# Kernel tuning notes

Hardware: AMD Instinct MI355X
Metric: run time of the kernel (lower is better)

Reference implementation:

```python
import jax, jax.numpy as jnp
import numpy as np

B, IN, OUT, NC, S = 4096, 512, 512, 64, 1


def setup_inputs() -> dict:
    key = jax.random.key(0)
    k = jax.random.split(key, 5)
    x = jax.random.normal(k[0], (B, IN), dtype=jnp.float32)
    centers = jax.random.normal(k[1], (NC, IN), dtype=jnp.float32)
    log_sigma = jnp.zeros((NC,), dtype=jnp.float32)
    coeff_mean = jax.random.normal(k[2], (IN, OUT, NC), dtype=jnp.float32) * 0.05
    coeff_log_var = jnp.full((IN, OUT, NC), -5.0, dtype=jnp.float32)
    base_weight = jax.random.normal(k[3], (IN, OUT), dtype=jnp.float32) * 0.05
    eps = jax.random.normal(k[4], (S, IN, OUT, NC), dtype=jnp.float32)
    return {"x": x, "centers": centers, "log_sigma": log_sigma,
            "coeff_mean": coeff_mean, "coeff_log_var": coeff_log_var,
            "base_weight": base_weight, "eps": eps}


def reference(x, centers, log_sigma, coeff_mean, coeff_log_var, base_weight, eps):
    # RBF basis: (B, NC). Original repeats this along in_features, but the
    # einsum 'bin,ion->bo' with an i-constant basis equals rbf @ coeffs.sum(i).
    dist_sq = jnp.sum((x[:, None, :] - centers[None, :, :]) ** 2, axis=-1)  # (B, NC)
    sigma = jnp.exp(log_sigma)  # (NC,)
    rbf = jnp.exp(-dist_sq / (2.0 * sigma ** 2 + 1e-8))  # (B, NC)

    # Sampled variational coefficients, reparameterized.
    std = jnp.exp(0.5 * coeff_log_var)
    coeffs = coeff_mean + eps * std            # (S, IN, OUT, NC)
    c_sum = coeffs.sum(axis=1)                 # (S, OUT, NC): sum over in_features
    n_samples = eps.shape[0]
    rbf_out = jnp.einsum('bn,son->bo', rbf, c_sum) / n_samples  # mean over samples

    out = rbf_out + x @ base_weight

    # KL vs N(0, 1) prior (prior_scale = 1.0): log(var/prior_var) = coeff_log_var
    var = jnp.exp(coeff_log_var)
    kl = 0.5 * jnp.sum(var + coeff_mean ** 2 - 1.0 - coeff_log_var)
    return out, kl
```

## Files before the change

kernel.cpp:

```cpp
#include <hip/hip_runtime.h>
#include <hip/hip_bf16.h>

#define B_SZ  4096
#define IN_F  512
#define OUT_F 512
#define NC    64
#define PAIRS 32768
#define TOT   (IN_F * PAIRS)
#define KTOT  (IN_F + NC)
#define RCH   32

typedef __attribute__((ext_vector_type(8))) short bf16x8;
typedef __attribute__((ext_vector_type(4))) float f32x4;

static __device__ inline unsigned short f2bf(float f) {
    __hip_bfloat16 h = __float2bfloat16(f);
    return *(unsigned short*)&h;
}

__global__ __launch_bounds__(512)
void k1_partial(const float* __restrict__ cm,
                const float* __restrict__ clv,
                const float* __restrict__ eps,
                float* __restrict__ part,
                float* __restrict__ klpart,
                int S) {
    int pb = blockIdx.x & 15;
    int rc = blockIdx.x >> 4;
    int p4 = pb * 2048 + (threadIdx.x << 2);
    float Sf = (float)S;

    f32x4 s = {0.f, 0.f, 0.f, 0.f};
    float klp = 0.f;

    for (int g = 0; g < 2; ++g) {
        size_t base = (size_t)(rc * 16 + g * 8) * PAIRS + p4;
        f32x4 M[8], LV[8], ES[8];
#pragma unroll
        for (int ii = 0; ii < 8; ++ii)
            M[ii] = __builtin_nontemporal_load((const f32x4*)(cm + base + (size_t)ii * PAIRS));
#pragma unroll
        for (int ii = 0; ii < 8; ++ii)
            LV[ii] = __builtin_nontemporal_load((const f32x4*)(clv + base + (size_t)ii * PAIRS));
#pragma unroll
        for (int ii = 0; ii < 8; ++ii)
            ES[ii] = __builtin_nontemporal_load((const f32x4*)(eps + base + (size_t)ii * PAIRS));
        for (int si = 1; si < S; ++si)
#pragma unroll
            for (int ii = 0; ii < 8; ++ii) {
                f32x4 e = __builtin_nontemporal_load(
                    (const f32x4*)(eps + (size_t)si * TOT + base + (size_t)ii * PAIRS));
                ES[ii] += e;
            }

#pragma unroll
        for (int ii = 0; ii < 8; ++ii) {
            float e1x = __expf(0.5f * LV[ii].x);
            float e1y = __expf(0.5f * LV[ii].y);
            float e1z = __expf(0.5f * LV[ii].z);
            float e1w = __expf(0.5f * LV[ii].w);
            s.x += Sf * M[ii].x + ES[ii].x * e1x;
            s.y += Sf * M[ii].y + ES[ii].y * e1y;
            s.z += Sf * M[ii].z + ES[ii].z * e1z;
            s.w += Sf * M[ii].w + ES[ii].w * e1w;
            klp += (e1x*e1x + M[ii].x*M[ii].x - 1.f - LV[ii].x);
            klp += (e1y*e1y + M[ii].y*M[ii].y - 1.f - LV[ii].y);
            klp += (e1z*e1z + M[ii].z*M[ii].z - 1.f - LV[ii].z);
            klp += (e1w*e1w + M[ii].w*M[ii].w - 1.f - LV[ii].w);
        }
    }

    *(f32x4*)(part + (size_t)rc * PAIRS + p4) = s;

    for (int off = 32; off; off >>= 1)
        klp += __shfl_down(klp, off, 64);
    __shared__ float wsum[8];
    if ((threadIdx.x & 63) == 0) wsum[threadIdx.x >> 6] = klp;
    __syncthreads();
    if (threadIdx.x == 0) {
        float t = 0.f;
#pragma unroll
        for (int i = 0; i < 8; ++i) t += wsum[i];
        klpart[blockIdx.x] = t;
    }
}

__global__ __launch_bounds__(512)
void k_mid(const float* __restrict__ x,
           const float* __restrict__ centers,
           const float* __restrict__ log_sigma,
           const float* __restrict__ part,
           const float* __restrict__ klpart,
           const float* __restrict__ bw,
           unsigned short* __restrict__ rbf,
           unsigned short* __restrict__ wct,
           unsigned short* __restrict__ xbf,
           float* __restrict__ kl_out,
           float inv_S) {
    __shared__ float shbuf[16 * 8 * 64];
    int bid = blockIdx.x, t = threadIdx.x;

    if (bid < 256) {
        float (*red)[8][64] = (float (*)[8][64])shbuf;
        int n = t & 63;
        int wu = __builtin_amdgcn_readfirstlane(t >> 6);
        int b0 = bid * 16;

        float creg[64];
#pragma unroll
        for (int q = 0; q < 16; ++q) {
            float4 v = *(const float4*)(centers + (size_t)n * IN_F + wu * 64 + q * 4);
            creg[q * 4 + 0] = v.x; creg[q * 4 + 1] = v.y;
            creg[q * 4 + 2] = v.z; creg[q * 4 + 3] = v.w;
        }

        float dacc[16];
#pragma unroll
        for (int bi = 0; bi < 16; ++bi) {
            const float* xr = x + (size_t)(b0 + bi) * IN_F + wu * 64;
            float d0 = 0.f, d1 = 0.f, d2 = 0.f, d3 = 0.f;
#pragma unroll
            for (int j = 0; j < 64; j += 4) {
                float t0 = xr[j + 0] - creg[j + 0];
                float t1 = xr[j + 1] - creg[j + 1];
                float t2 = xr[j + 2] - creg[j + 2];
                float t3 = xr[j + 3] - creg[j + 3];
                d0 = fmaf(t0, t0, d0); d1 = fmaf(t1, t1, d1);
                d2 = fmaf(t2, t2, d2); d3 = fmaf(t3, t3, d3);
            }
            dacc[bi] = (d0 + d1) + (d2 + d3);
        }
#pragma unroll
        for (int bi = 0; bi < 16; ++bi)
            red[bi][wu][n] = dacc[bi];
        __syncthreads();
#pragma unroll
        for (int pass = 0; pass < 2; ++pass) {
            int idx = pass * 512 + t;
            int bi = idx >> 6, nn = idx & 63;
            float ssum = 0.f;
#pragma unroll
            for (int w = 0; w < 8; ++w) ssum += red[bi][w][nn];
            float sg  = __expf(log_sigma[nn]);
            float inv = 1.f / (2.f * sg * sg + 1e-8f);
            rbf[(size_t)(b0 + bi) * NC + nn] = f2bf(__expf(-ssum * inv));
        }
    } else if (bid < 320) {
        int p = (bid - 256) * 512 + t;
        float a0 = 0.f, a1 = 0.f, a2 = 0.f, a3 = 0.f;
#pragma unroll
        for (int r = 0; r < RCH; r += 4) {
            a0 += part[(size_t)(r + 0) * PAIRS + p];
            a1 += part[(size_t)(r + 1) * PAIRS + p];
            a2 += part[(size_t)(r + 2) * PAIRS + p];
            a3 += part[(size_t)(r + 3) * PAIRS + p];
        }
        int o = p >> 6, n = p & 63;
        wct[(size_t)o * KTOT + IN_F + n] = f2bf(((a0 + a1) + (a2 + a3)) * inv_S);
    } else if (bid < 384) {
        float* tile = shbuf;
        int bb = bid - 320;
        int bi = bb >> 3, bj = bb & 7;
        int cq = t & 15, rq = t >> 4;
#pragma unroll
        for (int rr = 0; rr < 2; ++rr) {
            int row = rq * 2 + rr;
            float4 v = *(const float4*)(bw + (size_t)(bi * 64 + row) * OUT_F + bj * 64 + cq * 4);
            *(float4*)&tile[row * 68 + cq * 4] = v;
        }
        __syncthreads();
#pragma unroll
        for (int rr = 0; rr < 2; ++rr) {
            int orow = rq * 2 + rr;
            ushort4 w;
            w.x = f2bf(tile[(cq * 4 + 0) * 68 + orow]);
            w.y = f2bf(tile[(cq * 4 + 1) * 68 + orow]);
            w.z = f2bf(tile[(cq * 4 + 2) * 68 + orow]);
            w.w = f2bf(tile[(cq * 4 + 3) * 68 + orow]);
            *(ushort4*)(wct + (size_t)(bj * 64 + orow) * KTOT + bi * 64 + cq * 4) = w;
        }
    } else if (bid == 384) {
        float v = klpart[t];
        for (int off = 32; off; off >>= 1)
            v += __shfl_down(v, off, 64);
        float* wsum = shbuf;
        if ((t & 63) == 0) wsum[t >> 6] = v;
        __syncthreads();
        if (t == 0) {
            float s = 0.f;
#pragma unroll
            for (int i = 0; i < 8; ++i) s += wsum[i];
            kl_out[0] = 0.5f * s;
        }
    } else {
        size_t base = (size_t)(bid - 385) * 32768;
#pragma unroll
        for (int q = 0; q < 16; ++q) {
            size_t off = base + q * 2048 + t * 4;
            float4 v = *(const float4*)(x + off);
            ushort4 w = {f2bf(v.x), f2bf(v.y), f2bf(v.z), f2bf(v.w)};
            *(ushort4*)(xbf + off) = w;
        }
    }
}

__global__ __launch_bounds__(256)
void k3_mfma(const unsigned short* __restrict__ xbf,
             const unsigned short* __restrict__ rbf,
             const unsigned short* __restrict__ wct,
             float* __restrict__ out) {
    __shared__ __align__(16) unsigned short As[64 * 72];
    __shared__ __align__(16) unsigned short Bs[64 * 72];
    int t = threadIdx.x;
    int bm = blockIdx.x >> 3, bn = blockIdx.x & 7;
    int b0 = bm * 64, o0 = bn * 64;
    int ar = t & 63, ah = t >> 6;
    int lane = t & 63, wv = t >> 6;
    int fm = lane & 15, kg = lane >> 4;

    f32x4 acc[4] = {{0,0,0,0},{0,0,0,0},{0,0,0,0},{0,0,0,0}};
    const int abase = (wv * 16 + fm) * 72 + kg * 8;
    const int soff  = ar * 72 + ah * 16;

    for (int it = 0; it < 9; ++it) {
        bf16x8 av0, av1, bv0, bv1;
        if (it < 8) {
            int k0 = it * 64;
            av0 = *(const bf16x8*)(xbf + (size_t)(b0 + ar) * IN_F + k0 + ah * 16);
            av1 = *(const bf16x8*)(xbf + (size_t)(b0 + ar) * IN_F + k0 + ah * 16 + 8);
            bv0 = *(const bf16x8*)(wct + (size_t)(o0 + ar) * KTOT + k0 + ah * 16);
            bv1 = *(const bf16x8*)(wct + (size_t)(o0 + ar) * KTOT + k0 + ah * 16 + 8);
        } else {
            av0 = *(const bf16x8*)(rbf + (size_t)(b0 + ar) * NC + ah * 16);
            av1 = *(const bf16x8*)(rbf + (size_t)(b0 + ar) * NC + ah * 16 + 8);
            bv0 = *(const bf16x8*)(wct + (size_t)(o0 + ar) * KTOT + IN_F + ah * 16);
            bv1 = *(const bf16x8*)(wct + (size_t)(o0 + ar) * KTOT + IN_F + ah * 16 + 8);
        }
        __syncthreads();
        *(bf16x8*)&As[soff]     = av0;
        *(bf16x8*)&As[soff + 8] = av1;
        *(bf16x8*)&Bs[soff]     = bv0;
        *(bf16x8*)&Bs[soff + 8] = bv1;
        __syncthreads();
        bf16x8 af0 = *(bf16x8*)&As[abase];
        bf16x8 af1 = *(bf16x8*)&As[abase + 32];
#pragma unroll
        for (int nf = 0; nf < 4; ++nf) {
            bf16x8 b0f = *(bf16x8*)&Bs[(nf * 16 + fm) * 72 + kg * 8];
            acc[nf] = __builtin_amdgcn_mfma_f32_16x16x32_bf16(af0, b0f, acc[nf], 0, 0, 0);
            bf16x8 b1f = *(bf16x8*)&Bs[(nf * 16 + fm) * 72 + 32 + kg * 8];
            acc[nf] = __builtin_amdgcn_mfma_f32_16x16x32_bf16(af1, b1f, acc[nf], 0, 0, 0);
        }
    }

#pragma unroll
    for (int nf = 0; nf < 4; ++nf)
#pragma unroll
        for (int rr = 0; rr < 4; ++rr)
            out[(size_t)(b0 + wv * 16 + kg * 4 + rr) * OUT_F + o0 + nf * 16 + fm] = acc[nf][rr];
}

extern "C" void kernel_launch(void* const* d_in, const int* in_sizes, int n_in,
                              void* d_out, int out_size, void* d_ws, size_t ws_size,
                              hipStream_t stream) {
    const float* x         = (const float*)d_in[0];
    const float* centers   = (const float*)d_in[1];
    const float* log_sigma = (const float*)d_in[2];
    const float* cm        = (const float*)d_in[3];
    const float* clv       = (const float*)d_in[4];
    const float* bw        = (const float*)d_in[5];
    const float* eps       = (const float*)d_in[6];

    float* out = (float*)d_out;
    float* kl  = out + (size_t)B_SZ * OUT_F;

    float* part   = (float*)d_ws;
    float* klpart = part + (size_t)RCH * PAIRS;
    unsigned short* wct = (unsigned short*)(klpart + 512);
    unsigned short* rbf = wct + (size_t)OUT_F * KTOT;
    unsigned short* xbf = rbf + (size_t)B_SZ * NC;

    int S = in_sizes[6] / TOT;

    k1_partial<<<512, 512, 0, stream>>>(cm, clv, eps, part, klpart, S);
    k_mid<<<449, 512, 0, stream>>>(x, centers, log_sigma, part, klpart, bw,
                                   rbf, wct, xbf, kl, 1.0f / (float)S);
    k3_mfma<<<(B_SZ / 64) * (OUT_F / 64), 256, 0, stream>>>(xbf, rbf, wct, out);
}
```

Before: 234.2 us.

## Merge reduction and prep stages into two kernels with atomic-flag sync

The coefficient partial-sum kernel is fused with the independent RBF, base-weight transpose and x-to-bf16 conversion work into one 896-block launch, interleaving 4 reduction blocks with 3 prep blocks per group of 7. This lets the memory-heavy stream over the coefficient arrays overlap with the smaller prep tasks. The final partial-sum reduction and KL finalisation move into the first 64 blocks of the MFMA kernel. The other GEMM blocks run the base-weight K loop first and spin on an agent-scope atomic counter before the RBF K-chunk. This removes one launch but adds a spin-wait that relies on those 64 blocks being scheduled, a deadlock risk if residency were limited.

```diff
diff --git a/kernel.cpp b/kernel.cpp
--- a/kernel.cpp
+++ b/kernel.cpp
@@ -18,188 +18,165 @@
     return *(unsigned short*)&h;
 }
 
-__global__ __launch_bounds__(512)
-void k1_partial(const float* __restrict__ cm,
-                const float* __restrict__ clv,
-                const float* __restrict__ eps,
-                float* __restrict__ part,
-                float* __restrict__ klpart,
-                int S) {
-    int pb = blockIdx.x & 15;
-    int rc = blockIdx.x >> 4;
-    int p4 = pb * 2048 + (threadIdx.x << 2);
-    float Sf = (float)S;
-
-    f32x4 s = {0.f, 0.f, 0.f, 0.f};
-    float klp = 0.f;
-
-    for (int g = 0; g < 2; ++g) {
-        size_t base = (size_t)(rc * 16 + g * 8) * PAIRS + p4;
-        f32x4 M[8], LV[8], ES[8];
-#pragma unroll
-        for (int ii = 0; ii < 8; ++ii)
-            M[ii] = __builtin_nontemporal_load((const f32x4*)(cm + base + (size_t)ii * PAIRS));
-#pragma unroll
-        for (int ii = 0; ii < 8; ++ii)
-            LV[ii] = __builtin_nontemporal_load((const f32x4*)(clv + base + (size_t)ii * PAIRS));
-#pragma unroll
-        for (int ii = 0; ii < 8; ++ii)
-            ES[ii] = __builtin_nontemporal_load((const f32x4*)(eps + base + (size_t)ii * PAIRS));
-        for (int si = 1; si < S; ++si)
+__global__ __launch_bounds__(512, 4)
+void kA(const float* __restrict__ cm,
+        const float* __restrict__ clv,
+        const float* __restrict__ eps,
+        const float* __restrict__ x,
+        const float* __restrict__ centers,
+        const float* __restrict__ log_sigma,
+        const float* __restrict__ bw,
+        float* __restrict__ part,
+        float* __restrict__ klpart,
+        unsigned short* __restrict__ rbf,
+        unsigned short* __restrict__ wct,
+        unsigned short* __restrict__ xbf,
+        int* __restrict__ counter,
+        int S) {
+    __shared__ float shbuf[16 * 8 * 64];
+    int g7 = blockIdx.x / 7;
+    int r7 = blockIdx.x - g7 * 7;
+    int t  = threadIdx.x;
+
+    if (r7 < 4) {
+        int bid = g7 * 4 + r7;
+        int pb = bid & 15;
+        int rc = bid >> 4;
+        int p4 = pb * 2048 + (t << 2);
+        float Sf = (float)S;
+
+        f32x4 s = {0.f, 0.f, 0.f, 0.f};
+        float klp = 0.f;
+
+        for (int g = 0; g < 2; ++g) {
+            size_t base = (size_t)(rc * 16 + g * 8) * PAIRS + p4;
+            f32x4 M[8], LV[8], ES[8];
+#pragma unroll
+            for (int ii = 0; ii < 8; ++ii)
+                M[ii] = __builtin_nontemporal_load((const f32x4*)(cm + base + (size_t)ii * PAIRS));
+#pragma unroll
+            for (int ii = 0; ii < 8; ++ii)
+                LV[ii] = __builtin_nontemporal_load((const f32x4*)(clv + base + (size_t)ii * PAIRS));
+#pragma unroll
+            for (int ii = 0; ii < 8; ++ii)
+                ES[ii] = __builtin_nontemporal_load((const f32x4*)(eps + base + (size_t)ii * PAIRS));
+            for (int si = 1; si < S; ++si)
+#pragma unroll
+                for (int ii = 0; ii < 8; ++ii) {
+                    f32x4 e = __builtin_nontemporal_load(
+                        (const f32x4*)(eps + (size_t)si * TOT + base + (size_t)ii * PAIRS));
+                    ES[ii] += e;
+                }
+
 #pragma unroll
             for (int ii = 0; ii < 8; ++ii) {
-                f32x4 e = __builtin_nontemporal_load(
-                    (const f32x4*)(eps + (size_t)si * TOT + base + (size_t)ii * PAIRS));
-                ES[ii] += e;
-            }
-
-#pragma unroll
-        for (int ii = 0; ii < 8; ++ii) {
-            float e1x = __expf(0.5f * LV[ii].x);
-            float e1y = __expf(0.5f * LV[ii].y);
-            float e1z = __expf(0.5f * LV[ii].z);
-            float e1w = __expf(0.5f * LV[ii].w);
-            s.x += Sf * M[ii].x + ES[ii].x * e1x;
-            s.y += Sf * M[ii].y + ES[ii].y * e1y;
-            s.z += Sf * M[ii].z + ES[ii].z * e1z;
-            s.w += Sf * M[ii].w + ES[ii].w * e1w;
-            klp += (e1x*e1x + M[ii].x*M[ii].x - 1.f - LV[ii].x);
-            klp += (e1y*e1y + M[ii].y*M[ii].y - 1.f - LV[ii].y);
-            klp += (e1z*e1z + M[ii].z*M[ii].z - 1.f - LV[ii].z);
-            klp += (e1w*e1w + M[ii].w*M[ii].w - 1.f - LV[ii].w);
-        }
-    }
-
-    *(f32x4*)(part + (size_t)rc * PAIRS + p4) = s;
-
-    for (int off = 32; off; off >>= 1)
-        klp += __shfl_down(klp, off, 64);
-    __shared__ float wsum[8];
-    if ((threadIdx.x & 63) == 0) wsum[threadIdx.x >> 6] = klp;
-    __syncthreads();
-    if (threadIdx.x == 0) {
-        float t = 0.f;
-#pragma unroll
-        for (int i = 0; i < 8; ++i) t += wsum[i];
-        klpart[blockIdx.x] = t;
-    }
-}
-
-__global__ __launch_bounds__(512)
-void k_mid(const float* __restrict__ x,
-           const float* __restrict__ centers,
-           const float* __restrict__ log_sigma,
-           const float* __restrict__ part,
-           const float* __restrict__ klpart,
-           const float* __restrict__ bw,
-           unsigned short* __restrict__ rbf,
-           unsigned short* __restrict__ wct,
-           unsigned short* __restrict__ xbf,
-           float* __restrict__ kl_out,
-           float inv_S) {
-    __shared__ float shbuf[16 * 8 * 64];
-    int bid = blockIdx.x, t = threadIdx.x;
-
-    if (bid < 256) {
-        float (*red)[8][64] = (float (*)[8][64])shbuf;
-        int n = t & 63;
-        int wu = __builtin_amdgcn_readfirstlane(t >> 6);
-        int b0 = bid * 16;
-
-        float creg[64];
-#pragma unroll
-        for (int q = 0; q < 16; ++q) {
-            float4 v = *(const float4*)(centers + (size_t)n * IN_F + wu * 64 + q * 4);
-            creg[q * 4 + 0] = v.x; creg[q * 4 + 1] = v.y;
-            creg[q * 4 + 2] = v.z; creg[q * 4 + 3] = v.w;
-        }
-
-        float dacc[16];
-#pragma unroll
-        for (int bi = 0; bi < 16; ++bi) {
-            const float* xr = x + (size_t)(b0 + bi) * IN_F + wu * 64;
-            float d0 = 0.f, d1 = 0.f, d2 = 0.f, d3 = 0.f;
-#pragma unroll
-            for (int j = 0; j < 64; j += 4) {
-                float t0 = xr[j + 0] - creg[j + 0];
-                float t1 = xr[j + 1] - creg[j + 1];
-                float t2 = xr[j + 2] - creg[j + 2];
-                float t3 = xr[j + 3] - creg[j + 3];
-                d0 = fmaf(t0, t0, d0); d1 = fmaf(t1, t1, d1);
-                d2 = fmaf(t2, t2, d2); d3 = fmaf(t3, t3, d3);
-            }
-            dacc[bi] = (d0 + d1) + (d2 + d3);
-        }
-#pragma unroll
-        for (int bi = 0; bi < 16; ++bi)
-            red[bi][wu][n] = dacc[bi];
-        __syncthreads();
-#pragma unroll
-        for (int pass = 0; pass < 2; ++pass) {
-            int idx = pass * 512 + t;
-            int bi = idx >> 6, nn = idx & 63;
-            float ssum = 0.f;
-#pragma unroll
-            for (int w = 0; w < 8; ++w) ssum += red[bi][w][nn];
-            float sg  = __expf(log_sigma[nn]);
-            float inv = 1.f / (2.f * sg * sg + 1e-8f);
-            rbf[(size_t)(b0 + bi) * NC + nn] = f2bf(__expf(-ssum * inv));
-        }
-    } else if (bid < 320) {
-        int p = (bid - 256) * 512 + t;
-        float a0 = 0.f, a1 = 0.f, a2 = 0.f, a3 = 0.f;
-#pragma unroll
-        for (int r = 0; r < RCH; r += 4) {
-            a0 += part[(size_t)(r + 0) * PAIRS + p];
-            a1 += part[(size_t)(r + 1) * PAIRS + p];
-            a2 += part[(size_t)(r + 2) * PAIRS + p];
-            a3 += part[(size_t)(r + 3) * PAIRS + p];
-        }
-        int o = p >> 6, n = p & 63;
-        wct[(size_t)o * KTOT + IN_F + n] = f2bf(((a0 + a1) + (a2 + a3)) * inv_S);
-    } else if (bid < 384) {
-        float* tile = shbuf;
-        int bb = bid - 320;
-        int bi = bb >> 3, bj = bb & 7;
-        int cq = t & 15, rq = t >> 4;
-#pragma unroll
-        for (int rr = 0; rr < 2; ++rr) {
-            int row = rq * 2 + rr;
-            float4 v = *(const float4*)(bw + (size_t)(bi * 64 + row) * OUT_F + bj * 64 + cq * 4);
-            *(float4*)&tile[row * 68 + cq * 4] = v;
-        }
-        __syncthreads();
-#pragma unroll
-        for (int rr = 0; rr < 2; ++rr) {
-            int orow = rq * 2 + rr;
-            ushort4 w;
-            w.x = f2bf(tile[(cq * 4 + 0) * 68 + orow]);
-            w.y = f2bf(tile[(cq * 4 + 1) * 68 + orow]);
-            w.z = f2bf(tile[(cq * 4 + 2) * 68 + orow]);
-            w.w = f2bf(tile[(cq * 4 + 3) * 68 + orow]);
-            *(ushort4*)(wct + (size_t)(bj * 64 + orow) * KTOT + bi * 64 + cq * 4) = w;
-        }
-    } else if (bid == 384) {
-        float v = klpart[t];
+                float e1x = __expf(0.5f * LV[ii].x);
+                float e1y = __expf(0.5f * LV[ii].y);
+                float e1z = __expf(0.5f * LV[ii].z);
+                float e1w = __expf(0.5f * LV[ii].w);
+                s.x += Sf * M[ii].x + ES[ii].x * e1x;
+                s.y += Sf * M[ii].y + ES[ii].y * e1y;
+                s.z += Sf * M[ii].z + ES[ii].z * e1z;
+                s.w += Sf * M[ii].w + ES[ii].w * e1w;
+                klp += (e1x*e1x + M[ii].x*M[ii].x - 1.f - LV[ii].x);
+                klp += (e1y*e1y + M[ii].y*M[ii].y - 1.f - LV[ii].y);
+                klp += (e1z*e1z + M[ii].z*M[ii].z - 1.f - LV[ii].z);
+                klp += (e1w*e1w + M[ii].w*M[ii].w - 1.f - LV[ii].w);
+            }
+        }
+
+        *(f32x4*)(part + (size_t)rc * PAIRS + p4) = s;
+
         for (int off = 32; off; off >>= 1)
-            v += __shfl_down(v, off, 64);
+            klp += __shfl_down(klp, off, 64);
         float* wsum = shbuf;
-        if ((t & 63) == 0) wsum[t >> 6] = v;
+        if ((t & 63) == 0) wsum[t >> 6] = klp;
         __syncthreads();
         if (t == 0) {
-            float s = 0.f;
-#pragma unroll
-            for (int i = 0; i < 8; ++i) s += wsum[i];
-            kl_out[0] = 0.5f * s;
+            float tt = 0.f;
+#pragma unroll
+            for (int i = 0; i < 8; ++i) tt += wsum[i];
+            klpart[bid] = tt;
         }
     } else {
-        size_t base = (size_t)(bid - 385) * 32768;
-#pragma unroll
-        for (int q = 0; q < 16; ++q) {
-            size_t off = base + q * 2048 + t * 4;
-            float4 v = *(const float4*)(x + off);
-            ushort4 w = {f2bf(v.x), f2bf(v.y), f2bf(v.z), f2bf(v.w)};
-            *(ushort4*)(xbf + off) = w;
+        int e = g7 * 3 + (r7 - 4);
+        if (e < 256) {
+            if (e == 0 && t == 0) *counter = 0;
+            float (*red)[8][64] = (float (*)[8][64])shbuf;
+            int n = t & 63;
+            int wu = __builtin_amdgcn_readfirstlane(t >> 6);
+            int b0 = e * 16;
+
+            float creg[64];
+#pragma unroll
+            for (int q = 0; q < 16; ++q) {
+                float4 v = *(const float4*)(centers + (size_t)n * IN_F + wu * 64 + q * 4);
+                creg[q * 4 + 0] = v.x; creg[q * 4 + 1] = v.y;
+                creg[q * 4 + 2] = v.z; creg[q * 4 + 3] = v.w;
+            }
+
+            float dacc[16];
+#pragma unroll
+            for (int bi = 0; bi < 16; ++bi) {
+                const float* xr = x + (size_t)(b0 + bi) * IN_F + wu * 64;
+                float d0 = 0.f, d1 = 0.f, d2 = 0.f, d3 = 0.f;
+#pragma unroll
+                for (int j = 0; j < 64; j += 4) {
+                    float t0 = xr[j + 0] - creg[j + 0];
+                    float t1 = xr[j + 1] - creg[j + 1];
+                    float t2 = xr[j + 2] - creg[j + 2];
+                    float t3 = xr[j + 3] - creg[j + 3];
+                    d0 = fmaf(t0, t0, d0); d1 = fmaf(t1, t1, d1);
+                    d2 = fmaf(t2, t2, d2); d3 = fmaf(t3, t3, d3);
+                }
+                dacc[bi] = (d0 + d1) + (d2 + d3);
+            }
+#pragma unroll
+            for (int bi = 0; bi < 16; ++bi)
+                red[bi][wu][n] = dacc[bi];
+            __syncthreads();
+#pragma unroll
+            for (int pass = 0; pass < 2; ++pass) {
+                int idx = pass * 512 + t;
+                int bi = idx >> 6, nn = idx & 63;
+                float ssum = 0.f;
+#pragma unroll
+                for (int w = 0; w < 8; ++w) ssum += red[bi][w][nn];
+                float sg  = __expf(log_sigma[nn]);
+                float inv = 1.f / (2.f * sg * sg + 1e-8f);
+                rbf[(size_t)(b0 + bi) * NC + nn] = f2bf(__expf(-ssum * inv));
+            }
+        } else if (e < 320) {
+            float* tile = shbuf;
+            int bb = e - 256;
+            int bi = bb >> 3, bj = bb & 7;
+            int cq = t & 15, rq = t >> 4;
+#pragma unroll
+            for (int rr = 0; rr < 2; ++rr) {
+                int row = rq * 2 + rr;
+                float4 v = *(const float4*)(bw + (size_t)(bi * 64 + row) * OUT_F + bj * 64 + cq * 4);
+                *(float4*)&tile[row * 68 + cq * 4] = v;
+            }
+            __syncthreads();
+#pragma unroll
+            for (int rr = 0; rr < 2; ++rr) {
+                int orow = rq * 2 + rr;
+                ushort4 w;
+                w.x = f2bf(tile[(cq * 4 + 0) * 68 + orow]);
+                w.y = f2bf(tile[(cq * 4 + 1) * 68 + orow]);
+                w.z = f2bf(tile[(cq * 4 + 2) * 68 + orow]);
+                w.w = f2bf(tile[(cq * 4 + 3) * 68 + orow]);
+                *(ushort4*)(wct + (size_t)(bj * 64 + orow) * KTOT + bi * 64 + cq * 4) = w;
+            }
+        } else {
+            size_t base = (size_t)(e - 320) * 32768;
+#pragma unroll
+            for (int q = 0; q < 16; ++q) {
+                size_t off = base + q * 2048 + t * 4;
+                float4 v = *(const float4*)(x + off);
+                ushort4 w = {f2bf(v.x), f2bf(v.y), f2bf(v.z), f2bf(v.w)};
+                *(ushort4*)(xbf + off) = w;
+            }
         }
     }
 }
@@ -207,12 +184,50 @@
 __global__ __launch_bounds__(256)
 void k3_mfma(const unsigned short* __restrict__ xbf,
              const unsigned short* __restrict__ rbf,
-             const unsigned short* __restrict__ wct,
-             float* __restrict__ out) {
+             unsigned short* __restrict__ wct,
+             const float* __restrict__ part,
+             const float* __restrict__ klpart,
+             float* __restrict__ out,
+             float* __restrict__ kl_out,
+             int* __restrict__ counter,
+             float inv_S) {
     __shared__ __align__(16) unsigned short As[64 * 72];
     __shared__ __align__(16) unsigned short Bs[64 * 72];
+    __shared__ float klw[4];
     int t = threadIdx.x;
-    int bm = blockIdx.x >> 3, bn = blockIdx.x & 7;
+    int bid = blockIdx.x;
+
+    if (bid < 64) {
+#pragma unroll
+        for (int rep = 0; rep < 2; ++rep) {
+            int p = bid * 512 + rep * 256 + t;
+            float a0 = 0.f, a1 = 0.f, a2 = 0.f, a3 = 0.f;
+#pragma unroll
+            for (int r = 0; r < RCH; r += 4) {
+                a0 += part[(size_t)(r + 0) * PAIRS + p];
+                a1 += part[(size_t)(r + 1) * PAIRS + p];
+                a2 += part[(size_t)(r + 2) * PAIRS + p];
+                a3 += part[(size_t)(r + 3) * PAIRS + p];
+            }
+            wct[(size_t)(p >> 6) * KTOT + IN_F + (p & 63)] =
+                f2bf(((a0 + a1) + (a2 + a3)) * inv_S);
+        }
+        if (bid == 0) {
+            float v = klpart[t] + klpart[t + 256];
+            for (int off = 32; off; off >>= 1)
+                v += __shfl_down(v, off, 64);
+            if ((t & 63) == 0) klw[t >> 6] = v;
+            __syncthreads();
+            if (t == 0)
+                kl_out[0] = 0.5f * (klw[0] + klw[1] + klw[2] + klw[3]);
+        }
+        __threadfence();
+        __syncthreads();
+        if (t == 0)
+            __hip_atomic_fetch_add(counter, 1, __ATOMIC_RELEASE, __HIP_MEMORY_SCOPE_AGENT);
+    }
+
+    int bm = bid >> 3, bn = bid & 7;
     int b0 = bm * 64, o0 = bn * 64;
     int ar = t & 63, ah = t >> 6;
     int lane = t & 63, wv = t >> 6;
@@ -223,6 +238,13 @@
     const int soff  = ar * 72 + ah * 16;
 
     for (int it = 0; it < 9; ++it) {
+        if (it == 8) {
+            if (t == 0) {
+                while (__hip_atomic_load(counter, __ATOMIC_ACQUIRE,
+                                         __HIP_MEMORY_SCOPE_AGENT) < 64) {}
+            }
+            __syncthreads();
+        }
         bf16x8 av0, av1, bv0, bv1;
         if (it < 8) {
             int k0 = it * 64;
@@ -279,11 +301,12 @@
     unsigned short* wct = (unsigned short*)(klpart + 512);
     unsigned short* rbf = wct + (size_t)OUT_F * KTOT;
     unsigned short* xbf = rbf + (size_t)B_SZ * NC;
+    int* counter = (int*)(xbf + (size_t)B_SZ * IN_F);
 
     int S = in_sizes[6] / TOT;
 
-    k1_partial<<<512, 512, 0, stream>>>(cm, clv, eps, part, klpart, S);
-    k_mid<<<449, 512, 0, stream>>>(x, centers, log_sigma, part, klpart, bw,
-                                   rbf, wct, xbf, kl, 1.0f / (float)S);
-    k3_mfma<<<(B_SZ / 64) * (OUT_F / 64), 256, 0, stream>>>(xbf, rbf, wct, out);
+    kA<<<896, 512, 0, stream>>>(cm, clv, eps, x, centers, log_sigma, bw,
+                                part, klpart, rbf, wct, xbf, counter, S);
+    k3_mfma<<<512, 256, 0, stream>>>(xbf, rbf, wct, part, klpart,
+                                     out, kl, counter, 1.0f / (float)S);
 }
```

Measured after the change: 241.1 us. 2.9% more time.

## Move RBF computation into GEMM kernel with atomic counter handoff and fuse x bf16 conversion

Applied to the files above, without the earlier changes.

The RBF basis computation moves out of the middle kernel into the GEMM kernel. The first 256 blocks compute RBF and signal an atomic counter, and the GEMM blocks spin on that counter before the final RBF k-step. The separate x-to-bf16 conversion pass is removed; GEMM blocks load fp32 x and convert to bf16 in registers. This cuts an extra write and read of the bf16 copy of x and lets RBF work overlap with the GEMM. In exchange, x is read as fp32 repeatedly across the output-column tiles, and the spin-wait assumes the RBF blocks get scheduled before the waiting blocks.

```diff
diff --git a/kernel.cpp b/kernel.cpp
--- a/kernel.cpp
+++ b/kernel.cpp
@@ -86,67 +86,18 @@
 }
 
 __global__ __launch_bounds__(512)
-void k_mid(const float* __restrict__ x,
-           const float* __restrict__ centers,
-           const float* __restrict__ log_sigma,
-           const float* __restrict__ part,
-           const float* __restrict__ klpart,
-           const float* __restrict__ bw,
-           unsigned short* __restrict__ rbf,
-           unsigned short* __restrict__ wct,
-           unsigned short* __restrict__ xbf,
-           float* __restrict__ kl_out,
-           float inv_S) {
-    __shared__ float shbuf[16 * 8 * 64];
+void k_mid2(const float* __restrict__ part,
+            const float* __restrict__ klpart,
+            const float* __restrict__ bw,
+            unsigned short* __restrict__ wct,
+            float* __restrict__ kl_out,
+            int* __restrict__ counter,
+            float inv_S) {
+    __shared__ float shbuf[64 * 68];
     int bid = blockIdx.x, t = threadIdx.x;
 
-    if (bid < 256) {
-        float (*red)[8][64] = (float (*)[8][64])shbuf;
-        int n = t & 63;
-        int wu = __builtin_amdgcn_readfirstlane(t >> 6);
-        int b0 = bid * 16;
-
-        float creg[64];
-#pragma unroll
-        for (int q = 0; q < 16; ++q) {
-            float4 v = *(const float4*)(centers + (size_t)n * IN_F + wu * 64 + q * 4);
-            creg[q * 4 + 0] = v.x; creg[q * 4 + 1] = v.y;
-            creg[q * 4 + 2] = v.z; creg[q * 4 + 3] = v.w;
-        }
-
-        float dacc[16];
-#pragma unroll
-        for (int bi = 0; bi < 16; ++bi) {
-            const float* xr = x + (size_t)(b0 + bi) * IN_F + wu * 64;
-            float d0 = 0.f, d1 = 0.f, d2 = 0.f, d3 = 0.f;
-#pragma unroll
-            for (int j = 0; j < 64; j += 4) {
-                float t0 = xr[j + 0] - creg[j + 0];
-                float t1 = xr[j + 1] - creg[j + 1];
-                float t2 = xr[j + 2] - creg[j + 2];
-                float t3 = xr[j + 3] - creg[j + 3];
-                d0 = fmaf(t0, t0, d0); d1 = fmaf(t1, t1, d1);
-                d2 = fmaf(t2, t2, d2); d3 = fmaf(t3, t3, d3);
-            }
-            dacc[bi] = (d0 + d1) + (d2 + d3);
-        }
-#pragma unroll
-        for (int bi = 0; bi < 16; ++bi)
-            red[bi][wu][n] = dacc[bi];
-        __syncthreads();
-#pragma unroll
-        for (int pass = 0; pass < 2; ++pass) {
-            int idx = pass * 512 + t;
-            int bi = idx >> 6, nn = idx & 63;
-            float ssum = 0.f;
-#pragma unroll
-            for (int w = 0; w < 8; ++w) ssum += red[bi][w][nn];
-            float sg  = __expf(log_sigma[nn]);
-            float inv = 1.f / (2.f * sg * sg + 1e-8f);
-            rbf[(size_t)(b0 + bi) * NC + nn] = f2bf(__expf(-ssum * inv));
-        }
-    } else if (bid < 320) {
-        int p = (bid - 256) * 512 + t;
+    if (bid < 64) {
+        int p = bid * 512 + t;
         float a0 = 0.f, a1 = 0.f, a2 = 0.f, a3 = 0.f;
 #pragma unroll
         for (int r = 0; r < RCH; r += 4) {
@@ -157,9 +108,9 @@
         }
         int o = p >> 6, n = p & 63;
         wct[(size_t)o * KTOT + IN_F + n] = f2bf(((a0 + a1) + (a2 + a3)) * inv_S);
-    } else if (bid < 384) {
+    } else if (bid < 128) {
         float* tile = shbuf;
-        int bb = bid - 320;
+        int bb = bid - 64;
         int bi = bb >> 3, bj = bb & 7;
         int cq = t & 15, rq = t >> 4;
 #pragma unroll
@@ -179,7 +130,8 @@
             w.w = f2bf(tile[(cq * 4 + 3) * 68 + orow]);
             *(ushort4*)(wct + (size_t)(bj * 64 + orow) * KTOT + bi * 64 + cq * 4) = w;
         }
-    } else if (bid == 384) {
+    } else {
+        if (t == 0) *counter = 0;
         float v = klpart[t];
         for (int off = 32; off; off >>= 1)
             v += __shfl_down(v, off, 64);
@@ -192,27 +144,78 @@
             for (int i = 0; i < 8; ++i) s += wsum[i];
             kl_out[0] = 0.5f * s;
         }
-    } else {
-        size_t base = (size_t)(bid - 385) * 32768;
-#pragma unroll
-        for (int q = 0; q < 16; ++q) {
-            size_t off = base + q * 2048 + t * 4;
-            float4 v = *(const float4*)(x + off);
-            ushort4 w = {f2bf(v.x), f2bf(v.y), f2bf(v.z), f2bf(v.w)};
-            *(ushort4*)(xbf + off) = w;
-        }
     }
 }
 
 __global__ __launch_bounds__(256)
-void k3_mfma(const unsigned short* __restrict__ xbf,
-             const unsigned short* __restrict__ rbf,
-             const unsigned short* __restrict__ wct,
-             float* __restrict__ out) {
+void k3_fused(const float* __restrict__ x,
+              const float* __restrict__ centers,
+              const float* __restrict__ log_sigma,
+              const unsigned short* __restrict__ wct,
+              unsigned short* __restrict__ rbf,
+              float* __restrict__ out,
+              int* __restrict__ counter) {
     __shared__ __align__(16) unsigned short As[64 * 72];
     __shared__ __align__(16) unsigned short Bs[64 * 72];
+    __shared__ float red[16][4][64];
     int t = threadIdx.x;
-    int bm = blockIdx.x >> 3, bn = blockIdx.x & 7;
+    int bid = blockIdx.x;
+
+    if (bid < 256) {
+        int n = t & 63;
+        int wu = t >> 6;
+        int b0 = bid * 16;
+
+        float dacc[16];
+#pragma unroll
+        for (int bi = 0; bi < 16; ++bi) dacc[bi] = 0.f;
+
+        for (int h = 0; h < 2; ++h) {
+            float creg[64];
+#pragma unroll
+            for (int q = 0; q < 16; ++q) {
+                float4 v = *(const float4*)(centers + (size_t)n * IN_F + wu * 128 + h * 64 + q * 4);
+                creg[q * 4 + 0] = v.x; creg[q * 4 + 1] = v.y;
+                creg[q * 4 + 2] = v.z; creg[q * 4 + 3] = v.w;
+            }
+#pragma unroll
+            for (int bi = 0; bi < 16; ++bi) {
+                const float* xr = x + (size_t)(b0 + bi) * IN_F + wu * 128 + h * 64;
+                float d0 = 0.f, d1 = 0.f, d2 = 0.f, d3 = 0.f;
+#pragma unroll
+                for (int j = 0; j < 64; j += 4) {
+                    float t0 = xr[j + 0] - creg[j + 0];
+                    float t1 = xr[j + 1] - creg[j + 1];
+                    float t2 = xr[j + 2] - creg[j + 2];
+                    float t3 = xr[j + 3] - creg[j + 3];
+                    d0 = fmaf(t0, t0, d0); d1 = fmaf(t1, t1, d1);
+                    d2 = fmaf(t2, t2, d2); d3 = fmaf(t3, t3, d3);
+                }
+                dacc[bi] += (d0 + d1) + (d2 + d3);
+            }
+        }
+#pragma unroll
+        for (int bi = 0; bi < 16; ++bi)
+            red[bi][wu][n] = dacc[bi];
+        __syncthreads();
+#pragma unroll
+        for (int pass = 0; pass < 4; ++pass) {
+            int idx = pass * 256 + t;
+            int bi = idx >> 6, nn = idx & 63;
+            float ssum = red[bi][0][nn] + red[bi][1][nn] + red[bi][2][nn] + red[bi][3][nn];
+            float sg  = __expf(log_sigma[nn]);
+            float inv = 1.f / (2.f * sg * sg + 1e-8f);
+            rbf[(size_t)(b0 + bi) * NC + nn] = f2bf(__expf(-ssum * inv));
+        }
+        __threadfence();
+        __syncthreads();
+        if (t == 0)
+            __hip_atomic_fetch_add(counter, 1, __ATOMIC_RELEASE, __HIP_MEMORY_SCOPE_AGENT);
+        return;
+    }
+
+    int gb = bid - 256;
+    int bm = gb >> 3, bn = gb & 7;
     int b0 = bm * 64, o0 = bn * 64;
     int ar = t & 63, ah = t >> 6;
     int lane = t & 63, wv = t >> 6;
@@ -223,11 +226,29 @@
     const int soff  = ar * 72 + ah * 16;
 
     for (int it = 0; it < 9; ++it) {
+        if (it == 8) {
+            if (t == 0) {
+                while (__hip_atomic_load(counter, __ATOMIC_ACQUIRE,
+                                         __HIP_MEMORY_SCOPE_AGENT) < 256) {}
+            }
+            __syncthreads();
+        }
         bf16x8 av0, av1, bv0, bv1;
         if (it < 8) {
             int k0 = it * 64;
-            av0 = *(const bf16x8*)(xbf + (size_t)(b0 + ar) * IN_F + k0 + ah * 16);
-            av1 = *(const bf16x8*)(xbf + (size_t)(b0 + ar) * IN_F + k0 + ah * 16 + 8);
+            const float* xp = x + (size_t)(b0 + ar) * IN_F + k0 + ah * 16;
+            f32x4 a0 = *(const f32x4*)(xp);
+            f32x4 a1 = *(const f32x4*)(xp + 4);
+            f32x4 a2 = *(const f32x4*)(xp + 8);
+            f32x4 a3 = *(const f32x4*)(xp + 12);
+            av0[0] = (short)f2bf(a0.x); av0[1] = (short)f2bf(a0.y);
+            av0[2] = (short)f2bf(a0.z); av0[3] = (short)f2bf(a0.w);
+            av0[4] = (short)f2bf(a1.x); av0[5] = (short)f2bf(a1.y);
+            av0[6] = (short)f2bf(a1.z); av0[7] = (short)f2bf(a1.w);
+            av1[0] = (short)f2bf(a2.x); av1[1] = (short)f2bf(a2.y);
+            av1[2] = (short)f2bf(a2.z); av1[3] = (short)f2bf(a2.w);
+            av1[4] = (short)f2bf(a3.x); av1[5] = (short)f2bf(a3.y);
+            av1[6] = (short)f2bf(a3.z); av1[7] = (short)f2bf(a3.w);
             bv0 = *(const bf16x8*)(wct + (size_t)(o0 + ar) * KTOT + k0 + ah * 16);
             bv1 = *(const bf16x8*)(wct + (size_t)(o0 + ar) * KTOT + k0 + ah * 16 + 8);
         } else {
@@ -278,12 +299,13 @@
     float* klpart = part + (size_t)RCH * PAIRS;
     unsigned short* wct = (unsigned short*)(klpart + 512);
     unsigned short* rbf = wct + (size_t)OUT_F * KTOT;
-    unsigned short* xbf = rbf + (size_t)B_SZ * NC;
+    int* counter = (int*)(rbf + (size_t)B_SZ * NC);
 
     int S = in_sizes[6] / TOT;
 
     k1_partial<<<512, 512, 0, stream>>>(cm, clv, eps, part, klpart, S);
-    k_mid<<<449, 512, 0, stream>>>(x, centers, log_sigma, part, klpart, bw,
-                                   rbf, wct, xbf, kl, 1.0f / (float)S);
-    k3_mfma<<<(B_SZ / 64) * (OUT_F / 64), 256, 0, stream>>>(xbf, rbf, wct, out);
-}
+    k_mid2<<<129, 512, 0, stream>>>(part, klpart, bw, wct, kl, counter,
+                                    1.0f / (float)S);
+    k3_fused<<<768, 256, 0, stream>>>(x, centers, log_sigma, wct, rbf,
+                                      out, counter);
+}
```

New measurement: 281.2 us. +20.0%, slower.

## Compute RBF distances via bf16 MFMA norm expansion and fuse x conversion

Applied to the files above, without the earlier changes.

Replaces the direct scalar squared-distance loop with the expansion ||x||^2 + ||c||^2 - 2 x·c, computing x·c with bf16 MFMA on 64-row tiles. The bf16 conversion of x is folded into the same pass, which removes the separate conversion blocks and shrinks the grid from 449 to 193 blocks. This cuts the FP32 ALU work in the mid kernel and avoids reading x twice. The cost is precision: the bf16 dot product inside the expansion can suffer cancellation, which affects the exponentiated distances, and fewer blocks share the work.

```diff
diff --git a/kernel.cpp b/kernel.cpp
--- a/kernel.cpp
+++ b/kernel.cpp
@@ -86,67 +86,121 @@
 }
 
 __global__ __launch_bounds__(512)
-void k_mid(const float* __restrict__ x,
-           const float* __restrict__ centers,
-           const float* __restrict__ log_sigma,
-           const float* __restrict__ part,
-           const float* __restrict__ klpart,
-           const float* __restrict__ bw,
-           unsigned short* __restrict__ rbf,
-           unsigned short* __restrict__ wct,
-           unsigned short* __restrict__ xbf,
-           float* __restrict__ kl_out,
-           float inv_S) {
-    __shared__ float shbuf[16 * 8 * 64];
+void k_mid3(const float* __restrict__ x,
+            const float* __restrict__ centers,
+            const float* __restrict__ log_sigma,
+            const float* __restrict__ part,
+            const float* __restrict__ klpart,
+            const float* __restrict__ bw,
+            unsigned short* __restrict__ rbf,
+            unsigned short* __restrict__ wct,
+            unsigned short* __restrict__ xbf,
+            float* __restrict__ kl_out,
+            float inv_S) {
+    __shared__ __align__(16) float shbuf[5312];
     int bid = blockIdx.x, t = threadIdx.x;
 
-    if (bid < 256) {
-        float (*red)[8][64] = (float (*)[8][64])shbuf;
-        int n = t & 63;
-        int wu = __builtin_amdgcn_readfirstlane(t >> 6);
-        int b0 = bid * 16;
-
-        float creg[64];
-#pragma unroll
-        for (int q = 0; q < 16; ++q) {
-            float4 v = *(const float4*)(centers + (size_t)n * IN_F + wu * 64 + q * 4);
-            creg[q * 4 + 0] = v.x; creg[q * 4 + 1] = v.y;
-            creg[q * 4 + 2] = v.z; creg[q * 4 + 3] = v.w;
-        }
-
-        float dacc[16];
-#pragma unroll
-        for (int bi = 0; bi < 16; ++bi) {
-            const float* xr = x + (size_t)(b0 + bi) * IN_F + wu * 64;
-            float d0 = 0.f, d1 = 0.f, d2 = 0.f, d3 = 0.f;
+    if (bid < 64) {
+        unsigned short* As = (unsigned short*)shbuf;
+        unsigned short* Cs = (unsigned short*)(shbuf + 2304);
+        float* scr = shbuf + 4608;
+        float* cn  = shbuf + 5120;
+        float* inv = shbuf + 5184;
+        float* xnf = shbuf + 5248;
+
+        int b0 = bid * 64;
+
+        {
+            int n = t & 63, p = t >> 6;
+            const float* cp = centers + (size_t)n * IN_F + p * 64;
+            float s0 = 0.f, s1 = 0.f, s2 = 0.f, s3 = 0.f;
 #pragma unroll
             for (int j = 0; j < 64; j += 4) {
-                float t0 = xr[j + 0] - creg[j + 0];
-                float t1 = xr[j + 1] - creg[j + 1];
-                float t2 = xr[j + 2] - creg[j + 2];
-                float t3 = xr[j + 3] - creg[j + 3];
-                d0 = fmaf(t0, t0, d0); d1 = fmaf(t1, t1, d1);
-                d2 = fmaf(t2, t2, d2); d3 = fmaf(t3, t3, d3);
+                float4 v = *(const float4*)(cp + j);
+                s0 = fmaf(v.x, v.x, s0); s1 = fmaf(v.y, v.y, s1);
+                s2 = fmaf(v.z, v.z, s2); s3 = fmaf(v.w, v.w, s3);
             }
-            dacc[bi] = (d0 + d1) + (d2 + d3);
-        }
-#pragma unroll
-        for (int bi = 0; bi < 16; ++bi)
-            red[bi][wu][n] = dacc[bi];
-        __syncthreads();
-#pragma unroll
-        for (int pass = 0; pass < 2; ++pass) {
-            int idx = pass * 512 + t;
-            int bi = idx >> 6, nn = idx & 63;
-            float ssum = 0.f;
-#pragma unroll
-            for (int w = 0; w < 8; ++w) ssum += red[bi][w][nn];
-            float sg  = __expf(log_sigma[nn]);
-            float inv = 1.f / (2.f * sg * sg + 1e-8f);
-            rbf[(size_t)(b0 + bi) * NC + nn] = f2bf(__expf(-ssum * inv));
-        }
-    } else if (bid < 320) {
-        int p = (bid - 256) * 512 + t;
+            scr[p * 64 + n] = (s0 + s1) + (s2 + s3);
+        }
+        __syncthreads();
+        if (t < 64) {
+            float s = 0.f;
+#pragma unroll
+            for (int p = 0; p < 8; ++p) s += scr[p * 64 + t];
+            cn[t] = s;
+            float sg = __expf(log_sigma[t]);
+            inv[t] = 1.f / (2.f * sg * sg + 1e-8f);
+        }
+        __syncthreads();
+
+        int ar = t >> 3, ah = t & 7;
+        int lane = t & 63, wv = t >> 6;
+        int fm = lane & 15, kg = lane >> 4;
+        float xacc = 0.f;
+        f32x4 acc[4] = {{0,0,0,0},{0,0,0,0},{0,0,0,0},{0,0,0,0}};
+
+        for (int it = 0; it < 8; ++it) {
+            int k0 = it * 64;
+            const float* xp = x + (size_t)(b0 + ar) * IN_F + k0 + ah * 8;
+            f32x4 v0 = *(const f32x4*)(xp);
+            f32x4 v1 = *(const f32x4*)(xp + 4);
+            const float* cp = centers + (size_t)ar * IN_F + k0 + ah * 8;
+            f32x4 c0 = *(const f32x4*)(cp);
+            f32x4 c1 = *(const f32x4*)(cp + 4);
+            bf16x8 xb, cb;
+            xb[0] = (short)f2bf(v0.x); xb[1] = (short)f2bf(v0.y);
+            xb[2] = (short)f2bf(v0.z); xb[3] = (short)f2bf(v0.w);
+            xb[4] = (short)f2bf(v1.x); xb[5] = (short)f2bf(v1.y);
+            xb[6] = (short)f2bf(v1.z); xb[7] = (short)f2bf(v1.w);
+            cb[0] = (short)f2bf(c0.x); cb[1] = (short)f2bf(c0.y);
+            cb[2] = (short)f2bf(c0.z); cb[3] = (short)f2bf(c0.w);
+            cb[4] = (short)f2bf(c1.x); cb[5] = (short)f2bf(c1.y);
+            cb[6] = (short)f2bf(c1.z); cb[7] = (short)f2bf(c1.w);
+            xacc += v0.x*v0.x + v0.y*v0.y + v0.z*v0.z + v0.w*v0.w
+                  + v1.x*v1.x + v1.y*v1.y + v1.z*v1.z + v1.w*v1.w;
+            __syncthreads();
+            *(bf16x8*)&As[ar * 72 + ah * 8] = xb;
+            *(bf16x8*)&Cs[ar * 72 + ah * 8] = cb;
+            *(bf16x8*)(xbf + (size_t)(b0 + ar) * IN_F + k0 + ah * 8) = xb;
+            __syncthreads();
+            if (wv < 4) {
+                bf16x8 af0 = *(bf16x8*)&As[(wv * 16 + fm) * 72 + kg * 8];
+                bf16x8 af1 = *(bf16x8*)&As[(wv * 16 + fm) * 72 + 32 + kg * 8];
+#pragma unroll
+                for (int nf = 0; nf < 4; ++nf) {
+                    bf16x8 b0f = *(bf16x8*)&Cs[(nf * 16 + fm) * 72 + kg * 8];
+                    acc[nf] = __builtin_amdgcn_mfma_f32_16x16x32_bf16(af0, b0f, acc[nf], 0, 0, 0);
+                    bf16x8 b1f = *(bf16x8*)&Cs[(nf * 16 + fm) * 72 + 32 + kg * 8];
+                    acc[nf] = __builtin_amdgcn_mfma_f32_16x16x32_bf16(af1, b1f, acc[nf], 0, 0, 0);
+                }
+            }
+        }
+
+        scr[ar * 8 + ah] = xacc;
+        __syncthreads();
+        if (t < 64) {
+            float s = 0.f;
+#pragma unroll
+            for (int p = 0; p < 8; ++p) s += scr[t * 8 + p];
+            xnf[t] = s;
+        }
+        __syncthreads();
+
+        if (wv < 4) {
+#pragma unroll
+            for (int nf = 0; nf < 4; ++nf) {
+                int c = nf * 16 + fm;
+                float cnc = cn[c], ivc = inv[c];
+#pragma unroll
+                for (int rr = 0; rr < 4; ++rr) {
+                    int r = wv * 16 + kg * 4 + rr;
+                    float d = xnf[r] + cnc - 2.f * acc[nf][rr];
+                    rbf[(size_t)(b0 + r) * NC + c] = f2bf(__expf(-d * ivc));
+                }
+            }
+        }
+    } else if (bid < 128) {
+        int p = (bid - 64) * 512 + t;
         float a0 = 0.f, a1 = 0.f, a2 = 0.f, a3 = 0.f;
 #pragma unroll
         for (int r = 0; r < RCH; r += 4) {
@@ -157,9 +211,9 @@
         }
         int o = p >> 6, n = p & 63;
         wct[(size_t)o * KTOT + IN_F + n] = f2bf(((a0 + a1) + (a2 + a3)) * inv_S);
-    } else if (bid < 384) {
+    } else if (bid < 192) {
         float* tile = shbuf;
-        int bb = bid - 320;
+        int bb = bid - 128;
         int bi = bb >> 3, bj = bb & 7;
         int cq = t & 15, rq = t >> 4;
 #pragma unroll
@@ -179,7 +233,7 @@
             w.w = f2bf(tile[(cq * 4 + 3) * 68 + orow]);
             *(ushort4*)(wct + (size_t)(bj * 64 + orow) * KTOT + bi * 64 + cq * 4) = w;
         }
-    } else if (bid == 384) {
+    } else {
         float v = klpart[t];
         for (int off = 32; off; off >>= 1)
             v += __shfl_down(v, off, 64);
@@ -191,15 +245,6 @@
 #pragma unroll
             for (int i = 0; i < 8; ++i) s += wsum[i];
             kl_out[0] = 0.5f * s;
-        }
-    } else {
-        size_t base = (size_t)(bid - 385) * 32768;
-#pragma unroll
-        for (int q = 0; q < 16; ++q) {
-            size_t off = base + q * 2048 + t * 4;
-            float4 v = *(const float4*)(x + off);
-            ushort4 w = {f2bf(v.x), f2bf(v.y), f2bf(v.z), f2bf(v.w)};
-            *(ushort4*)(xbf + off) = w;
         }
     }
 }
@@ -283,7 +328,7 @@
     int S = in_sizes[6] / TOT;
 
     k1_partial<<<512, 512, 0, stream>>>(cm, clv, eps, part, klpart, S);
-    k_mid<<<449, 512, 0, stream>>>(x, centers, log_sigma, part, klpart, bw,
-                                   rbf, wct, xbf, kl, 1.0f / (float)S);
+    k_mid3<<<193, 512, 0, stream>>>(x, centers, log_sigma, part, klpart, bw,
+                                    rbf, wct, xbf, kl, 1.0f / (float)S);
     k3_mfma<<<(B_SZ / 64) * (OUT_F / 64), 256, 0, stream>>>(xbf, rbf, wct, out);
 }
```

Result: faster. 225.8 us (-3.6%).
